# Optimization experiments

Hardware: AMD Instinct MI355X
Metric: run time of the kernel (lower is better)

The kernel has to match this reference:

```python
import jax, jax.numpy as jnp
import numpy as np

B, L, D_IN = 2048, 512, 32
PRED_LEN = 96
COND = 128      # cond_dim (z_dim)
XPROJ = 128     # x_proj_dim defaults to cond_dim
ODE_H = 128     # ode_hidden
TDIM = 128      # time_dim
HID = 256       # hidden of final MLP
N_STEPS = 32    # fixed-step RK4 steps over t in [0,1] (stands in for adaptive dopri5)
LN_EPS = 1e-5


def _linear(x, w, b):
    return x @ w.T + b


def _layernorm(x, g, b):
    mu = jnp.mean(x, axis=-1, keepdims=True)
    var = jnp.var(x, axis=-1, keepdims=True)
    return (x - mu) * jax.lax.rsqrt(var + LN_EPS) * g + b


def _interp(x_seq, t):
    # linear interp over sequence dim: x_seq (B,L,D), scalar t in [0,1] -> (B,D)
    Ls = x_seq.shape[1]
    pos = jnp.clip(t, 0.0, 1.0) * (Ls - 1)
    i0 = jnp.clip(jnp.floor(pos).astype(jnp.int32), 0, Ls - 1)
    i1 = jnp.clip(i0 + 1, 0, Ls - 1)
    w = (pos - i0.astype(pos.dtype))
    x0 = jax.lax.dynamic_index_in_dim(x_seq, i0, axis=1, keepdims=False)
    x1 = jax.lax.dynamic_index_in_dim(x_seq, i1, axis=1, keepdims=False)
    return (1.0 - w) * x0 + w * x1


def setup_inputs() -> dict:
    key = jax.random.key(0)
    ks = jax.random.split(key, 16)

    def kaiming(k, shape):
        return jax.random.normal(k, shape, jnp.float32) * np.float32(np.sqrt(2.0 / shape[-1]))

    IN_F = PRED_LEN * D_IN + COND + TDIM   # 3328
    OUT_F = PRED_LEN * D_IN                # 3072
    return {
        "x_t": jax.random.normal(ks[0], (B, PRED_LEN, D_IN), jnp.float32),
        "past": jax.random.normal(ks[1], (B, L, D_IN), jnp.float32),
        "t": jax.random.randint(ks[2], (B,), 0, 1000),
        "xproj_w": kaiming(ks[3], (XPROJ, D_IN)), "xproj_b": jnp.zeros((XPROJ,), jnp.float32),
        "z0_w": kaiming(ks[4], (COND, XPROJ)), "z0_b": jnp.zeros((COND,), jnp.float32),
        "ln_g": jnp.ones((COND,), jnp.float32), "ln_b": jnp.zeros((COND,), jnp.float32),
        "w1": kaiming(ks[5], (ODE_H, COND + XPROJ)), "b1": jnp.zeros((ODE_H,), jnp.float32),
        "w2": kaiming(ks[6], (ODE_H, ODE_H)), "b2": jnp.zeros((ODE_H,), jnp.float32),
        "w3": kaiming(ks[7], (COND, ODE_H)), "b3": jnp.zeros((COND,), jnp.float32),
        "fw1": kaiming(ks[8], (HID, IN_F)), "fb1": jnp.zeros((HID,), jnp.float32),
        "fw2": kaiming(ks[9], (HID, HID)), "fb2": jnp.zeros((HID,), jnp.float32),
        "fw3": kaiming(ks[10], (OUT_F, HID)), "fb3": jnp.zeros((OUT_F,), jnp.float32),
    }


def _time_emb(t):
    half = TDIM // 2
    freqs = jnp.exp(-np.float32(np.log(10000.0)) * jnp.arange(half, dtype=jnp.float32) / (half - 1))
    args = t.astype(jnp.float32)[:, None] * freqs[None, :]
    return jnp.concatenate([jnp.sin(args), jnp.cos(args)], axis=1)  # (B, TDIM)


def _forward(x_t, past, t, xproj_w, xproj_b, z0_w, z0_b, ln_g, ln_b,
             w1, b1, w2, b2, w3, b3, fw1, fb1, fw2, fb2, fw3, fb3):
    Bn = x_t.shape[0]
    x_seq = _linear(past, xproj_w, xproj_b)           # (B,L,XPROJ)
    z0 = _linear(x_seq[:, 0, :], z0_w, z0_b)          # (B,COND)

    def odef(tt, z):
        xt = _interp(x_seq, tt)                       # (B,XPROJ)
        zn = _layernorm(z, ln_g, ln_b)
        h = jnp.concatenate([zn, xt], axis=-1)
        h = jax.nn.silu(_linear(h, w1, b1))
        h = jax.nn.silu(_linear(h, w2, b2))
        return _linear(h, w3, b3)                     # (B,COND)

    dt = jnp.float32(1.0 / N_STEPS)

    def step(z, tt):
        k1 = odef(tt, z)
        k2 = odef(tt + dt * 0.5, z + dt * 0.5 * k1)
        k3 = odef(tt + dt * 0.5, z + dt * 0.5 * k2)
        k4 = odef(tt + dt, z + dt * k3)
        return z + (dt / 6.0) * (k1 + 2.0 * k2 + 2.0 * k3 + k4), None

    ts = jnp.arange(N_STEPS, dtype=jnp.float32) * dt
    cond, _ = jax.lax.scan(step, z0, ts)              # zT (B,COND)

    temb = _time_emb(t)                               # (B,TDIM)
    x_flat = x_t.reshape(Bn, -1)                      # (B,PRED_LEN*D_IN)
    h = jnp.concatenate([x_flat, cond, temb], axis=1)
    h = jax.nn.silu(_linear(h, fw1, fb1))
    h = jax.nn.silu(_linear(h, fw2, fb2))
    eps = _linear(h, fw3, fb3)
    return eps.reshape(Bn, PRED_LEN, D_IN)


def reference(x_t, past, t, xproj_w, xproj_b, z0_w, z0_b, ln_g, ln_b,
              w1, b1, w2, b2, w3, b3, fw1, fb1, fw2, fb2, fw3, fb3):
    return _forward(x_t, past, t, xproj_w, xproj_b, z0_w, z0_b, ln_g, ln_b,
                    w1, b1, w2, b2, w3, b3, fw1, fb1, fw2, fb2, fw3, fb3)
```

## Files before the change

kernel.cpp:

```cpp
#include <hip/hip_runtime.h>
#include <math.h>

typedef _Float16 h8f16 __attribute__((ext_vector_type(8)));
typedef _Float16 h4f16 __attribute__((ext_vector_type(4)));
typedef float f32x4 __attribute__((ext_vector_type(4)));

#define MFMA16(a, b, c) __builtin_amdgcn_mfma_f32_16x16x32_f16((a), (b), (c), 0, 0, 0)

__device__ __forceinline__ float silu_f(float v) {
    return v * __builtin_amdgcn_rcpf(1.0f + __expf(-v));
}

__global__ __launch_bounds__(128) void z0_kernel(
    const float* __restrict__ past,
    const float* __restrict__ xw, const float* __restrict__ xb,
    const float* __restrict__ zw, const float* __restrict__ zb,
    float* __restrict__ zbuf)
{
    __shared__ float p[32];
    __shared__ float x0[128];
    const int b = blockIdx.x;
    const int tid = threadIdx.x;
    if (tid < 32) p[tid] = past[(long)b * 512 * 32 + tid];
    __syncthreads();
    float s = xb[tid];
#pragma unroll
    for (int c = 0; c < 32; ++c) s += p[c] * xw[tid * 32 + c];
    x0[tid] = s;
    __syncthreads();
    float z = zb[tid];
    for (int k = 0; k < 128; ++k) z += x0[k] * zw[tid * 128 + k];
    zbuf[(long)b * 128 + tid] = z;
}

__global__ __launch_bounds__(256, 1) void ode_kernel(
    const float* __restrict__ past,
    const float* __restrict__ xproj_w, const float* __restrict__ xproj_b,
    const float* __restrict__ ln_g, const float* __restrict__ ln_b,
    const float* __restrict__ w1, const float* __restrict__ b1,
    const float* __restrict__ w2, const float* __restrict__ b2,
    const float* __restrict__ w3, const float* __restrict__ b3,
    float* __restrict__ zbuf)
{
    __shared__ _Float16 bxAll[65][16][40];
    __shared__ _Float16 hbuf[16][136];
    __shared__ _Float16 h1buf[16][136];
    __shared__ _Float16 h2buf[16][136];
    __shared__ float zS[16][132];
    __shared__ float kS[16][132];

    const int tid  = threadIdx.x;
    const int lane = tid & 63;
    const int wq   = tid >> 6;
    const int lrow = lane & 15;
    const int lhi  = lane >> 4;
    const int b0   = blockIdx.x * 16;

    h8f16 w1f[2][4], wcf[2], w2f[2][4], w3f[2][4];
    float b1t[2], b2r[2], b3r[2];
#pragma unroll
    for (int nt = 0; nt < 2; ++nt) {
        const int n = wq * 32 + nt * 16 + lrow;
#pragma unroll
        for (int ks = 0; ks < 4; ++ks) {
            const float* s = w1 + n * 256 + ks * 32 + lhi * 8;
            h8f16 v;
#pragma unroll
            for (int j = 0; j < 8; ++j) v[j] = (_Float16)s[j];
            w1f[nt][ks] = v;
        }
        {
            float wc[8] = {0, 0, 0, 0, 0, 0, 0, 0};
            float bc = 0.0f;
            const int c0 = lhi * 8;
            const float* w1b = w1 + n * 256 + 128;
#pragma unroll 4
            for (int k = 0; k < 128; ++k) {
                const float a = w1b[k];
                bc += a * xproj_b[k];
                const float* xr = xproj_w + k * 32 + c0;
#pragma unroll
                for (int j = 0; j < 8; ++j) wc[j] += a * xr[j];
            }
            h8f16 v;
#pragma unroll
            for (int j = 0; j < 8; ++j) v[j] = (_Float16)wc[j];
            wcf[nt] = v;
            b1t[nt] = b1[n] + bc;
        }
#pragma unroll
        for (int ks = 0; ks < 4; ++ks) {
            const float* s2 = w2 + n * 128 + ks * 32 + lhi * 8;
            const float* s3 = w3 + n * 128 + ks * 32 + lhi * 8;
            h8f16 v2, v3;
#pragma unroll
            for (int j = 0; j < 8; ++j) { v2[j] = (_Float16)s2[j]; v3[j] = (_Float16)s3[j]; }
            w2f[nt][ks] = v2; w3f[nt][ks] = v3;
        }
        b2r[nt] = b2[n]; b3r[nt] = b3[n];
    }

    const int r8 = tid >> 4;
    const int c8 = (tid & 15) * 8;
    float gR[8], bR[8];
#pragma unroll
    for (int j = 0; j < 8; ++j) { gR[j] = ln_g[c8 + j]; bR[j] = ln_b[c8 + j]; }

    for (int flat = tid; flat < 65 * 128; flat += 256) {
        const int e  = flat >> 7;
        const int u  = flat & 127;
        const int r  = u >> 3;
        const int c  = (u & 7) * 4;
        const float pos = (float)e * 7.984375f;
        const int i0 = (int)pos;
        const int i1 = (i0 < 511) ? i0 + 1 : 511;
        const float w = pos - (float)i0;
        const f32x4 a0 = *(const f32x4*)(past + ((long)(b0 + r) * 512 + i0) * 32 + c);
        const f32x4 a1 = *(const f32x4*)(past + ((long)(b0 + r) * 512 + i1) * 32 + c);
        h4f16 v;
#pragma unroll
        for (int j = 0; j < 4; ++j) v[j] = (_Float16)((1.0f - w) * a0[j] + w * a1[j]);
        *(h4f16*)&bxAll[e][r][c] = v;
    }

#pragma unroll
    for (int j = 0; j < 8; ++j) {
        zS[r8][c8 + j] = zbuf[(long)(b0 + r8) * 128 + c8 + j];
        kS[r8][c8 + j] = 0.0f;
    }

    f32x4 krk[2];
    krk[0] = (f32x4){0, 0, 0, 0}; krk[1] = (f32x4){0, 0, 0, 0};
    const float DT = 1.0f / 32.0f;

    __syncthreads();

#pragma unroll 1
    for (int step = 0; step < 32; ++step) {
#pragma unroll 1
        for (int sub = 0; sub < 4; ++sub) {
            const int e = 2 * step + ((sub + 1) >> 1);
            const float cin = (sub == 0) ? 0.0f : (sub == 3) ? DT : 0.5f * DT;

            {
                float x[8];
                float sum = 0.f, sq = 0.f;
#pragma unroll
                for (int j = 0; j < 8; ++j) {
                    float v = zS[r8][c8 + j] + cin * kS[r8][c8 + j];
                    x[j] = v; sum += v; sq += v * v;
                }
#pragma unroll
                for (int m = 1; m < 16; m <<= 1) {
                    sum += __shfl_xor(sum, m, 16);
                    sq  += __shfl_xor(sq,  m, 16);
                }
                const float mu  = sum * (1.0f / 128.0f);
                const float var = sq * (1.0f / 128.0f) - mu * mu;
                const float inv = 1.0f / sqrtf(var + 1e-5f);
                h8f16 o;
#pragma unroll
                for (int j = 0; j < 8; ++j)
                    o[j] = (_Float16)((x[j] - mu) * inv * gR[j] + bR[j]);
                *(h8f16*)&hbuf[r8][c8] = o;
            }
            __syncthreads();

            {
                h8f16 az[4];
#pragma unroll
                for (int ks = 0; ks < 4; ++ks)
                    az[ks] = *(const h8f16*)&hbuf[lrow][ks * 32 + lhi * 8];
                const h8f16 bx = *(const h8f16*)&bxAll[e][lrow][lhi * 8];
                f32x4 a0 = {0, 0, 0, 0}, a1 = {0, 0, 0, 0};
#pragma unroll
                for (int ks = 0; ks < 4; ++ks) {
                    a0 = MFMA16(az[ks], w1f[0][ks], a0);
                    a1 = MFMA16(az[ks], w1f[1][ks], a1);
                }
                a0 = MFMA16(bx, wcf[0], a0);
                a1 = MFMA16(bx, wcf[1], a1);
#pragma unroll
                for (int j = 0; j < 4; ++j) {
                    h1buf[lhi * 4 + j][wq * 32 + lrow]      = (_Float16)silu_f(a0[j] + b1t[0]);
                    h1buf[lhi * 4 + j][wq * 32 + 16 + lrow] = (_Float16)silu_f(a1[j] + b1t[1]);
                }
            }
            __syncthreads();

            {
                f32x4 a0 = {0, 0, 0, 0}, a1 = {0, 0, 0, 0};
#pragma unroll
                for (int ks = 0; ks < 4; ++ks) {
                    h8f16 a = *(const h8f16*)&h1buf[lrow][ks * 32 + lhi * 8];
                    a0 = MFMA16(a, w2f[0][ks], a0);
                    a1 = MFMA16(a, w2f[1][ks], a1);
                }
#pragma unroll
                for (int j = 0; j < 4; ++j) {
                    h2buf[lhi * 4 + j][wq * 32 + lrow]      = (_Float16)silu_f(a0[j] + b2r[0]);
                    h2buf[lhi * 4 + j][wq * 32 + 16 + lrow] = (_Float16)silu_f(a1[j] + b2r[1]);
                }
            }
            __syncthreads();

            {
                f32x4 a0 = {0, 0, 0, 0}, a1 = {0, 0, 0, 0};
#pragma unroll
                for (int ks = 0; ks < 4; ++ks) {
                    h8f16 a = *(const h8f16*)&h2buf[lrow][ks * 32 + lhi * 8];
                    a0 = MFMA16(a, w3f[0][ks], a0);
                    a1 = MFMA16(a, w3f[1][ks], a1);
                }
                if (sub < 3) {
                    const float wgt = (sub == 0) ? 1.0f : 2.0f;
#pragma unroll
                    for (int j = 0; j < 4; ++j) {
                        const float k0v = a0[j] + b3r[0];
                        const float k1v = a1[j] + b3r[1];
                        kS[lhi * 4 + j][wq * 32 + lrow]      = k0v;
                        kS[lhi * 4 + j][wq * 32 + 16 + lrow] = k1v;
                        if (sub == 0) { krk[0][j] = k0v;        krk[1][j] = k1v; }
                        else          { krk[0][j] += wgt * k0v; krk[1][j] += wgt * k1v; }
                    }
                } else {
#pragma unroll
                    for (int j = 0; j < 4; ++j) {
                        const float k0v = a0[j] + b3r[0];
                        const float k1v = a1[j] + b3r[1];
                        const int rr = lhi * 4 + j;
                        zS[rr][wq * 32 + lrow]      += (DT / 6.0f) * (krk[0][j] + k0v);
                        zS[rr][wq * 32 + 16 + lrow] += (DT / 6.0f) * (krk[1][j] + k1v);
                    }
                }
            }
            __syncthreads();
        }
    }

#pragma unroll
    for (int j = 0; j < 8; ++j)
        zbuf[(long)(b0 + r8) * 128 + c8 + j] = zS[r8][c8 + j];
}

__global__ __launch_bounds__(256) void hcat_kernel(
    const float* __restrict__ x_t, const float* __restrict__ cond,
    const int* __restrict__ tvals, _Float16* __restrict__ hcat)
{
    const int gid = blockIdx.x * 256 + threadIdx.x;
    const int b  = gid / 416;
    const int j0 = (gid % 416) * 8;
    h8f16 v;
    if (j0 < 3072) {
        const float* s = x_t + (long)b * 3072 + j0;
#pragma unroll
        for (int j = 0; j < 8; ++j) v[j] = (_Float16)s[j];
    } else if (j0 < 3200) {
        const float* s = cond + (long)b * 128 + (j0 - 3072);
#pragma unroll
        for (int j = 0; j < 8; ++j) v[j] = (_Float16)s[j];
    } else {
        const float tv = (float)tvals[b];
#pragma unroll
        for (int j = 0; j < 8; ++j) {
            const int jj  = j0 - 3200 + j;
            const int idx = (jj < 64) ? jj : jj - 64;
            const float fr = expf(-9.210340371976184f * (float)idx * (1.0f / 63.0f));
            const float a  = tv * fr;
            v[j] = (_Float16)((jj < 64) ? sinf(a) : cosf(a));
        }
    }
    *(h8f16*)&hcat[(long)b * 3328 + j0] = v;
}

template <bool SILU, bool OUT_F16>
__global__ __launch_bounds__(256) void gemm_f16(
    const _Float16* __restrict__ A, const float* __restrict__ W,
    const float* __restrict__ bias, void* __restrict__ out,
    int M, int N, int K)
{
    __shared__ _Float16 aS[64][40];
    __shared__ _Float16 wS[64][40];
    const int mb = blockIdx.x * 64, nb = blockIdx.y * 64;
    const int tid = threadIdx.x, lane = tid & 63, wq = tid >> 6;
    const int lrow = lane & 15, lhi = lane >> 4;
    f32x4 acc[4];
#pragma unroll
    for (int nt = 0; nt < 4; ++nt) acc[nt] = (f32x4){0, 0, 0, 0};

    const int sr = tid >> 2;
    const int sk = (tid & 3) * 8;

    for (int k0 = 0; k0 < K; k0 += 32) {
        {
            h8f16 v = *(const h8f16*)&A[(long)(mb + sr) * K + k0 + sk];
            *(h8f16*)&aS[sr][sk] = v;
        }
        {
            const float* s = &W[(long)(nb + sr) * K + k0 + sk];
            h8f16 v;
#pragma unroll
            for (int j = 0; j < 8; ++j) v[j] = (_Float16)s[j];
            *(h8f16*)&wS[sr][sk] = v;
        }
        __syncthreads();
        h8f16 a = *(const h8f16*)&aS[wq * 16 + lrow][lhi * 8];
#pragma unroll
        for (int nt = 0; nt < 4; ++nt) {
            h8f16 bfr = *(const h8f16*)&wS[nt * 16 + lrow][lhi * 8];
            acc[nt] = MFMA16(a, bfr, acc[nt]);
        }
        __syncthreads();
    }

#pragma unroll
    for (int nt = 0; nt < 4; ++nt) {
        const int cc = nb + nt * 16 + lrow;
        const float bv = bias[cc];
#pragma unroll
        for (int j = 0; j < 4; ++j) {
            const int rr = mb + wq * 16 + lhi * 4 + j;
            float v = acc[nt][j] + bv;
            if (SILU) v = silu_f(v);
            if (OUT_F16) ((_Float16*)out)[(long)rr * N + cc] = (_Float16)v;
            else         ((float*)out)[(long)rr * N + cc] = v;
        }
    }
}

extern "C" void kernel_launch(void* const* d_in, const int* in_sizes, int n_in,
                              void* d_out, int out_size, void* d_ws, size_t ws_size,
                              hipStream_t stream)
{
    const float* x_t     = (const float*)d_in[0];
    const float* past    = (const float*)d_in[1];
    const int*   tvals   = (const int*)d_in[2];
    const float* xproj_w = (const float*)d_in[3];
    const float* xproj_b = (const float*)d_in[4];
    const float* z0_w    = (const float*)d_in[5];
    const float* z0_b    = (const float*)d_in[6];
    const float* ln_g    = (const float*)d_in[7];
    const float* ln_b    = (const float*)d_in[8];
    const float* w1      = (const float*)d_in[9];
    const float* b1      = (const float*)d_in[10];
    const float* w2      = (const float*)d_in[11];
    const float* b2      = (const float*)d_in[12];
    const float* w3      = (const float*)d_in[13];
    const float* b3      = (const float*)d_in[14];
    const float* fw1     = (const float*)d_in[15];
    const float* fb1     = (const float*)d_in[16];
    const float* fw2     = (const float*)d_in[17];
    const float* fb2     = (const float*)d_in[18];
    const float* fw3     = (const float*)d_in[19];
    const float* fb3     = (const float*)d_in[20];

    char* ws = (char*)d_ws;
    float*     zbuf = (float*)ws;
    _Float16*  hcat = (_Float16*)(ws + (1 << 20));
    _Float16*  h1   = (_Float16*)(ws + 15 * (1 << 20));
    _Float16*  h2   = (_Float16*)(ws + 16 * (1 << 20));

    z0_kernel<<<2048, 128, 0, stream>>>(past, xproj_w, xproj_b, z0_w, z0_b, zbuf);

    ode_kernel<<<128, 256, 0, stream>>>(past, xproj_w, xproj_b, ln_g, ln_b,
                                        w1, b1, w2, b2, w3, b3, zbuf);

    hcat_kernel<<<(2048 * 416) / 256, 256, 0, stream>>>(x_t, zbuf, tvals, hcat);

    gemm_f16<true,  true ><<<dim3(32, 4),  256, 0, stream>>>(hcat, fw1, fb1, h1, 2048, 256, 3328);
    gemm_f16<true,  true ><<<dim3(32, 4),  256, 0, stream>>>(h1,   fw2, fb2, h2, 2048, 256, 256);
    gemm_f16<false, false><<<dim3(32, 48), 256, 0, stream>>>(h2,   fw3, fb3, d_out, 2048, 3072, 256);
}
```

Before: 335.7 us.

## Fuse LayerNorm into ODE MFMA stage and read x_t directly in first GEMM

In the ODE kernel, the RK4 state now lives in registers (zc) instead of shared memory. The next ODE input is written to a single XOR-swizzled shared buffer, and the LayerNorm is computed inside the first MFMA stage. That removes one barrier per sub-step, and the h1/h2 buffers are also swizzled to avoid bank conflicts. The hcat concatenation kernel is replaced by a small cond/time-embedding buffer, so the first GEMM converts x_t from fp32 on the fly and skips writing and re-reading a large fp16 activation. The trade-off is more register pressure and a duplicated LayerNorm reduction across waves.

New measurement: 434.7 us. +29.5%, slower.

```diff
diff --git a/kernel.cpp b/kernel.cpp
--- a/kernel.cpp
+++ b/kernel.cpp
@@ -43,11 +43,9 @@
     float* __restrict__ zbuf)
 {
     __shared__ _Float16 bxAll[65][16][40];
-    __shared__ _Float16 hbuf[16][136];
-    __shared__ _Float16 h1buf[16][136];
-    __shared__ _Float16 h2buf[16][136];
-    __shared__ float zS[16][132];
-    __shared__ float kS[16][132];
+    __shared__ float    vS[16 * 128];
+    __shared__ _Float16 h1S[16 * 128];
+    __shared__ _Float16 h2S[16 * 128];
 
     const int tid  = threadIdx.x;
     const int lane = tid & 63;
@@ -55,6 +53,7 @@
     const int lrow = lane & 15;
     const int lhi  = lane >> 4;
     const int b0   = blockIdx.x * 16;
+    const int rsw  = lrow & 7;
 
     h8f16 w1f[2][4], wcf[2], w2f[2][4], w3f[2][4];
     float b1t[2], b2r[2], b3r[2];
@@ -100,11 +99,14 @@
         b2r[nt] = b2[n]; b3r[nt] = b3[n];
     }
 
-    const int r8 = tid >> 4;
-    const int c8 = (tid & 15) * 8;
-    float gR[8], bR[8];
-#pragma unroll
-    for (int j = 0; j < 8; ++j) { gR[j] = ln_g[c8 + j]; bR[j] = ln_b[c8 + j]; }
+    float gln[4][8], bln[4][8];
+#pragma unroll
+    for (int ks = 0; ks < 4; ++ks)
+#pragma unroll
+        for (int j = 0; j < 8; ++j) {
+            gln[ks][j] = ln_g[ks * 32 + lhi * 8 + j];
+            bln[ks][j] = ln_b[ks * 32 + lhi * 8 + j];
+        }
 
     for (int flat = tid; flat < 65 * 128; flat += 256) {
         const int e  = flat >> 7;
@@ -123,10 +125,21 @@
         *(h4f16*)&bxAll[e][r][c] = v;
     }
 
-#pragma unroll
-    for (int j = 0; j < 8; ++j) {
-        zS[r8][c8 + j] = zbuf[(long)(b0 + r8) * 128 + c8 + j];
-        kS[r8][c8 + j] = 0.0f;
+    const int cA = wq * 32 + lrow, cB = cA + 16;
+    float zc[2][4];
+#pragma unroll
+    for (int j = 0; j < 4; ++j) {
+        const long rb = (long)(b0 + 4 * lhi + j) * 128;
+        zc[0][j] = zbuf[rb + cA];
+        zc[1][j] = zbuf[rb + cB];
+    }
+#pragma unroll
+    for (int j = 0; j < 4; ++j) {
+        const int row = 4 * lhi + j;
+        const int sA = row * 128 + (((cA >> 2) ^ (row & 7)) << 2) + (cA & 3);
+        const int sB = row * 128 + (((cB >> 2) ^ (row & 7)) << 2) + (cB & 3);
+        vS[sA] = zc[0][j];
+        vS[sB] = zc[1][j];
     }
 
     f32x4 krk[2];
@@ -140,37 +153,43 @@
 #pragma unroll 1
         for (int sub = 0; sub < 4; ++sub) {
             const int e = 2 * step + ((sub + 1) >> 1);
-            const float cin = (sub == 0) ? 0.0f : (sub == 3) ? DT : 0.5f * DT;
 
             {
-                float x[8];
-                float sum = 0.f, sq = 0.f;
-#pragma unroll
-                for (int j = 0; j < 8; ++j) {
-                    float v = zS[r8][c8 + j] + cin * kS[r8][c8 + j];
-                    x[j] = v; sum += v; sq += v * v;
-                }
-#pragma unroll
-                for (int m = 1; m < 16; m <<= 1) {
-                    sum += __shfl_xor(sum, m, 16);
-                    sq  += __shfl_xor(sq,  m, 16);
-                }
-                const float mu  = sum * (1.0f / 128.0f);
-                const float var = sq * (1.0f / 128.0f) - mu * mu;
+                f32x4 va[4][2];
+#pragma unroll
+                for (int ks = 0; ks < 4; ++ks) {
+                    const int bA = (8 * ks + 2 * lhi) ^ rsw;
+                    const int bB = (8 * ks + 2 * lhi + 1) ^ rsw;
+                    va[ks][0] = *(const f32x4*)&vS[lrow * 128 + (bA << 2)];
+                    va[ks][1] = *(const f32x4*)&vS[lrow * 128 + (bB << 2)];
+                }
+                float s = 0.f, q = 0.f;
+#pragma unroll
+                for (int ks = 0; ks < 4; ++ks)
+#pragma unroll
+                    for (int h = 0; h < 2; ++h)
+#pragma unroll
+                        for (int j = 0; j < 4; ++j) {
+                            const float v = va[ks][h][j];
+                            s += v; q += v * v;
+                        }
+                s += __shfl_xor(s, 16); q += __shfl_xor(q, 16);
+                s += __shfl_xor(s, 32); q += __shfl_xor(q, 32);
+                const float mu  = s * (1.0f / 128.0f);
+                const float var = q * (1.0f / 128.0f) - mu * mu;
                 const float inv = 1.0f / sqrtf(var + 1e-5f);
-                h8f16 o;
-#pragma unroll
-                for (int j = 0; j < 8; ++j)
-                    o[j] = (_Float16)((x[j] - mu) * inv * gR[j] + bR[j]);
-                *(h8f16*)&hbuf[r8][c8] = o;
-            }
-            __syncthreads();
-
-            {
+
                 h8f16 az[4];
 #pragma unroll
-                for (int ks = 0; ks < 4; ++ks)
-                    az[ks] = *(const h8f16*)&hbuf[lrow][ks * 32 + lhi * 8];
+                for (int ks = 0; ks < 4; ++ks) {
+                    h8f16 o;
+#pragma unroll
+                    for (int j = 0; j < 8; ++j) {
+                        const float v = va[ks][j >> 2][j & 3];
+                        o[j] = (_Float16)((v - mu) * inv * gln[ks][j] + bln[ks][j]);
+                    }
+                    az[ks] = o;
+                }
                 const h8f16 bx = *(const h8f16*)&bxAll[e][lrow][lhi * 8];
                 f32x4 a0 = {0, 0, 0, 0}, a1 = {0, 0, 0, 0};
 #pragma unroll
@@ -182,8 +201,11 @@
                 a1 = MFMA16(bx, wcf[1], a1);
 #pragma unroll
                 for (int j = 0; j < 4; ++j) {
-                    h1buf[lhi * 4 + j][wq * 32 + lrow]      = (_Float16)silu_f(a0[j] + b1t[0]);
-                    h1buf[lhi * 4 + j][wq * 32 + 16 + lrow] = (_Float16)silu_f(a1[j] + b1t[1]);
+                    const int row = 4 * lhi + j;
+                    const int pA = row * 128 + ((((cA >> 3) ^ (row & 7)) << 3)) + (cA & 7);
+                    const int pB = row * 128 + ((((cB >> 3) ^ (row & 7)) << 3)) + (cB & 7);
+                    h1S[pA] = (_Float16)silu_f(a0[j] + b1t[0]);
+                    h1S[pB] = (_Float16)silu_f(a1[j] + b1t[1]);
                 }
             }
             __syncthreads();
@@ -192,14 +214,18 @@
                 f32x4 a0 = {0, 0, 0, 0}, a1 = {0, 0, 0, 0};
 #pragma unroll
                 for (int ks = 0; ks < 4; ++ks) {
-                    h8f16 a = *(const h8f16*)&h1buf[lrow][ks * 32 + lhi * 8];
+                    const int blk = (4 * ks + lhi) ^ rsw;
+                    h8f16 a = *(const h8f16*)&h1S[lrow * 128 + (blk << 3)];
                     a0 = MFMA16(a, w2f[0][ks], a0);
                     a1 = MFMA16(a, w2f[1][ks], a1);
                 }
 #pragma unroll
                 for (int j = 0; j < 4; ++j) {
-                    h2buf[lhi * 4 + j][wq * 32 + lrow]      = (_Float16)silu_f(a0[j] + b2r[0]);
-                    h2buf[lhi * 4 + j][wq * 32 + 16 + lrow] = (_Float16)silu_f(a1[j] + b2r[1]);
+                    const int row = 4 * lhi + j;
+                    const int pA = row * 128 + ((((cA >> 3) ^ (row & 7)) << 3)) + (cA & 7);
+                    const int pB = row * 128 + ((((cB >> 3) ^ (row & 7)) << 3)) + (cB & 7);
+                    h2S[pA] = (_Float16)silu_f(a0[j] + b2r[0]);
+                    h2S[pB] = (_Float16)silu_f(a1[j] + b2r[1]);
                 }
             }
             __syncthreads();
@@ -208,30 +234,39 @@
                 f32x4 a0 = {0, 0, 0, 0}, a1 = {0, 0, 0, 0};
 #pragma unroll
                 for (int ks = 0; ks < 4; ++ks) {
-                    h8f16 a = *(const h8f16*)&h2buf[lrow][ks * 32 + lhi * 8];
+                    const int blk = (4 * ks + lhi) ^ rsw;
+                    h8f16 a = *(const h8f16*)&h2S[lrow * 128 + (blk << 3)];
                     a0 = MFMA16(a, w3f[0][ks], a0);
                     a1 = MFMA16(a, w3f[1][ks], a1);
                 }
-                if (sub < 3) {
-                    const float wgt = (sub == 0) ? 1.0f : 2.0f;
-#pragma unroll
-                    for (int j = 0; j < 4; ++j) {
-                        const float k0v = a0[j] + b3r[0];
-                        const float k1v = a1[j] + b3r[1];
-                        kS[lhi * 4 + j][wq * 32 + lrow]      = k0v;
-                        kS[lhi * 4 + j][wq * 32 + 16 + lrow] = k1v;
-                        if (sub == 0) { krk[0][j] = k0v;        krk[1][j] = k1v; }
-                        else          { krk[0][j] += wgt * k0v; krk[1][j] += wgt * k1v; }
+#pragma unroll
+                for (int j = 0; j < 4; ++j) {
+                    const float k0v = a0[j] + b3r[0];
+                    const float k1v = a1[j] + b3r[1];
+                    float v0, v1;
+                    if (sub == 0) {
+                        krk[0][j] = k0v; krk[1][j] = k1v;
+                        v0 = zc[0][j] + 0.5f * DT * k0v;
+                        v1 = zc[1][j] + 0.5f * DT * k1v;
+                    } else if (sub == 1) {
+                        krk[0][j] += 2.0f * k0v; krk[1][j] += 2.0f * k1v;
+                        v0 = zc[0][j] + 0.5f * DT * k0v;
+                        v1 = zc[1][j] + 0.5f * DT * k1v;
+                    } else if (sub == 2) {
+                        krk[0][j] += 2.0f * k0v; krk[1][j] += 2.0f * k1v;
+                        v0 = zc[0][j] + DT * k0v;
+                        v1 = zc[1][j] + DT * k1v;
+                    } else {
+                        zc[0][j] += (DT / 6.0f) * (krk[0][j] + k0v);
+                        zc[1][j] += (DT / 6.0f) * (krk[1][j] + k1v);
+                        v0 = zc[0][j];
+                        v1 = zc[1][j];
                     }
-                } else {
-#pragma unroll
-                    for (int j = 0; j < 4; ++j) {
-                        const float k0v = a0[j] + b3r[0];
-                        const float k1v = a1[j] + b3r[1];
-                        const int rr = lhi * 4 + j;
-                        zS[rr][wq * 32 + lrow]      += (DT / 6.0f) * (krk[0][j] + k0v);
-                        zS[rr][wq * 32 + 16 + lrow] += (DT / 6.0f) * (krk[1][j] + k1v);
-                    }
+                    const int row = 4 * lhi + j;
+                    const int sA = row * 128 + (((cA >> 2) ^ (row & 7)) << 2) + (cA & 3);
+                    const int sB = row * 128 + (((cB >> 2) ^ (row & 7)) << 2) + (cB & 3);
+                    vS[sA] = v0;
+                    vS[sB] = v1;
                 }
             }
             __syncthreads();
@@ -239,38 +274,95 @@
     }
 
 #pragma unroll
-    for (int j = 0; j < 8; ++j)
-        zbuf[(long)(b0 + r8) * 128 + c8 + j] = zS[r8][c8 + j];
-}
-
-__global__ __launch_bounds__(256) void hcat_kernel(
-    const float* __restrict__ x_t, const float* __restrict__ cond,
-    const int* __restrict__ tvals, _Float16* __restrict__ hcat)
+    for (int j = 0; j < 4; ++j) {
+        const long rb = (long)(b0 + 4 * lhi + j) * 128;
+        zbuf[rb + cA] = zc[0][j];
+        zbuf[rb + cB] = zc[1][j];
+    }
+}
+
+__global__ __launch_bounds__(256) void cbuf_kernel(
+    const float* __restrict__ cond, const int* __restrict__ tvals,
+    _Float16* __restrict__ cbuf)
 {
     const int gid = blockIdx.x * 256 + threadIdx.x;
-    const int b  = gid / 416;
-    const int j0 = (gid % 416) * 8;
+    const int b  = gid >> 5;
+    const int j0 = (gid & 31) * 8;
     h8f16 v;
-    if (j0 < 3072) {
-        const float* s = x_t + (long)b * 3072 + j0;
-#pragma unroll
-        for (int j = 0; j < 8; ++j) v[j] = (_Float16)s[j];
-    } else if (j0 < 3200) {
-        const float* s = cond + (long)b * 128 + (j0 - 3072);
+    if (j0 < 128) {
+        const float* s = cond + (long)b * 128 + j0;
 #pragma unroll
         for (int j = 0; j < 8; ++j) v[j] = (_Float16)s[j];
     } else {
         const float tv = (float)tvals[b];
 #pragma unroll
         for (int j = 0; j < 8; ++j) {
-            const int jj  = j0 - 3200 + j;
+            const int jj  = j0 - 128 + j;
             const int idx = (jj < 64) ? jj : jj - 64;
             const float fr = expf(-9.210340371976184f * (float)idx * (1.0f / 63.0f));
             const float a  = tv * fr;
             v[j] = (_Float16)((jj < 64) ? sinf(a) : cosf(a));
         }
     }
-    *(h8f16*)&hcat[(long)b * 3328 + j0] = v;
+    *(h8f16*)&cbuf[(long)b * 256 + j0] = v;
+}
+
+__global__ __launch_bounds__(256) void gemm1_kernel(
+    const float* __restrict__ x_t, const _Float16* __restrict__ cbuf,
+    const float* __restrict__ W, const float* __restrict__ bias,
+    _Float16* __restrict__ out)
+{
+    const int M = 2048, N = 256, K = 3328;
+    __shared__ _Float16 aS[64][40];
+    __shared__ _Float16 wS[64][40];
+    const int mb = blockIdx.x * 64, nb = blockIdx.y * 64;
+    const int tid = threadIdx.x, lane = tid & 63, wq = tid >> 6;
+    const int lrow = lane & 15, lhi = lane >> 4;
+    f32x4 acc[4];
+#pragma unroll
+    for (int nt = 0; nt < 4; ++nt) acc[nt] = (f32x4){0, 0, 0, 0};
+
+    const int sr = tid >> 2;
+    const int sk = (tid & 3) * 8;
+
+    for (int k0 = 0; k0 < K; k0 += 32) {
+        if (k0 < 3072) {
+            const float* s = x_t + (long)(mb + sr) * 3072 + k0 + sk;
+            h8f16 v;
+#pragma unroll
+            for (int j = 0; j < 8; ++j) v[j] = (_Float16)s[j];
+            *(h8f16*)&aS[sr][sk] = v;
+        } else {
+            *(h8f16*)&aS[sr][sk] =
+                *(const h8f16*)&cbuf[(long)(mb + sr) * 256 + (k0 - 3072) + sk];
+        }
+        {
+            const float* s = &W[(long)(nb + sr) * K + k0 + sk];
+            h8f16 v;
+#pragma unroll
+            for (int j = 0; j < 8; ++j) v[j] = (_Float16)s[j];
+            *(h8f16*)&wS[sr][sk] = v;
+        }
+        __syncthreads();
+        h8f16 a = *(const h8f16*)&aS[wq * 16 + lrow][lhi * 8];
+#pragma unroll
+        for (int nt = 0; nt < 4; ++nt) {
+            h8f16 bfr = *(const h8f16*)&wS[nt * 16 + lrow][lhi * 8];
+            acc[nt] = MFMA16(a, bfr, acc[nt]);
+        }
+        __syncthreads();
+    }
+
+#pragma unroll
+    for (int nt = 0; nt < 4; ++nt) {
+        const int cc = nb + nt * 16 + lrow;
+        const float bv = bias[cc];
+#pragma unroll
+        for (int j = 0; j < 4; ++j) {
+            const int rr = mb + wq * 16 + lhi * 4 + j;
+            out[(long)rr * N + cc] = (_Float16)silu_f(acc[nt][j] + bv);
+        }
+    }
 }
 
 template <bool SILU, bool OUT_F16>
@@ -356,18 +448,18 @@
 
     char* ws = (char*)d_ws;
     float*     zbuf = (float*)ws;
-    _Float16*  hcat = (_Float16*)(ws + (1 << 20));
-    _Float16*  h1   = (_Float16*)(ws + 15 * (1 << 20));
-    _Float16*  h2   = (_Float16*)(ws + 16 * (1 << 20));
+    _Float16*  cbuf = (_Float16*)(ws + (1 << 20));
+    _Float16*  h1   = (_Float16*)(ws + 2 * (1 << 20));
+    _Float16*  h2   = (_Float16*)(ws + 3 * (1 << 20));
 
     z0_kernel<<<2048, 128, 0, stream>>>(past, xproj_w, xproj_b, z0_w, z0_b, zbuf);
 
     ode_kernel<<<128, 256, 0, stream>>>(past, xproj_w, xproj_b, ln_g, ln_b,
                                         w1, b1, w2, b2, w3, b3, zbuf);
 
-    hcat_kernel<<<(2048 * 416) / 256, 256, 0, stream>>>(x_t, zbuf, tvals, hcat);
-
-    gemm_f16<true,  true ><<<dim3(32, 4),  256, 0, stream>>>(hcat, fw1, fb1, h1, 2048, 256, 3328);
-    gemm_f16<true,  true ><<<dim3(32, 4),  256, 0, stream>>>(h1,   fw2, fb2, h2, 2048, 256, 256);
-    gemm_f16<false, false><<<dim3(32, 48), 256, 0, stream>>>(h2,   fw3, fb3, d_out, 2048, 3072, 256);
-}
+    cbuf_kernel<<<256, 256, 0, stream>>>(zbuf, tvals, cbuf);
+
+    gemm1_kernel<<<dim3(32, 4), 256, 0, stream>>>(x_t, cbuf, fw1, fb1, h1);
+    gemm_f16<true,  true ><<<dim3(32, 4),  256, 0, stream>>>(h1, fw2, fb2, h2, 2048, 256, 256);
+    gemm_f16<false, false><<<dim3(32, 48), 256, 0, stream>>>(h2, fw3, fb3, d_out, 2048, 3072, 256);
+}
```

## Fuse z0 into ODE kernel, widen to 8 waves, fold LN affine into W1

Applied to the files above, without the earlier changes.

The z0 projection kernel is merged into the ODE kernel, so one launch disappears. The block grows to 512 threads so each wave owns 16 output columns instead of 32, which halves the MFMA chain per wave. LayerNorm gamma/beta are folded into W1 and its bias, and normalisation is applied in fp16 on MFMA operands read straight from hbuf, which removes the separate LN phase and one barrier per substep. The state z and the RK accumulators now live in registers. The interpolated past rows are prefetched from global one substep ahead instead of being staged all at once into shared memory. The trade-offs are more fp16 rounding in the normalisation and the z0 work running on only 128 blocks.

After: 372.3 us. +10.9%, slower.

```diff
diff --git a/kernel.cpp b/kernel.cpp
--- a/kernel.cpp
+++ b/kernel.cpp
@@ -2,7 +2,6 @@
 #include <math.h>
 
 typedef _Float16 h8f16 __attribute__((ext_vector_type(8)));
-typedef _Float16 h4f16 __attribute__((ext_vector_type(4)));
 typedef float f32x4 __attribute__((ext_vector_type(4)));
 
 #define MFMA16(a, b, c) __builtin_amdgcn_mfma_f32_16x16x32_f16((a), (b), (c), 0, 0, 0)
@@ -11,236 +10,248 @@
     return v * __builtin_amdgcn_rcpf(1.0f + __expf(-v));
 }
 
-__global__ __launch_bounds__(128) void z0_kernel(
-    const float* __restrict__ past,
-    const float* __restrict__ xw, const float* __restrict__ xb,
-    const float* __restrict__ zw, const float* __restrict__ zb,
-    float* __restrict__ zbuf)
-{
-    __shared__ float p[32];
-    __shared__ float x0[128];
-    const int b = blockIdx.x;
-    const int tid = threadIdx.x;
-    if (tid < 32) p[tid] = past[(long)b * 512 * 32 + tid];
-    __syncthreads();
-    float s = xb[tid];
-#pragma unroll
-    for (int c = 0; c < 32; ++c) s += p[c] * xw[tid * 32 + c];
-    x0[tid] = s;
-    __syncthreads();
-    float z = zb[tid];
-    for (int k = 0; k < 128; ++k) z += x0[k] * zw[tid * 128 + k];
-    zbuf[(long)b * 128 + tid] = z;
-}
-
-__global__ __launch_bounds__(256, 1) void ode_kernel(
+__global__ __launch_bounds__(512, 1) void ode_kernel(
     const float* __restrict__ past,
     const float* __restrict__ xproj_w, const float* __restrict__ xproj_b,
+    const float* __restrict__ z0_w, const float* __restrict__ z0_b,
     const float* __restrict__ ln_g, const float* __restrict__ ln_b,
     const float* __restrict__ w1, const float* __restrict__ b1,
     const float* __restrict__ w2, const float* __restrict__ b2,
     const float* __restrict__ w3, const float* __restrict__ b3,
     float* __restrict__ zbuf)
 {
-    __shared__ _Float16 bxAll[65][16][40];
     __shared__ _Float16 hbuf[16][136];
-    __shared__ _Float16 h1buf[16][136];
-    __shared__ _Float16 h2buf[16][136];
-    __shared__ float zS[16][132];
-    __shared__ float kS[16][132];
+    __shared__ _Float16 h1S[16][136];
+    __shared__ _Float16 h2S[16][136];
+    __shared__ float    pS[16][33];
+    __shared__ float    x0S[16][128];
+    __shared__ float    zS0[16][129];
 
     const int tid  = threadIdx.x;
+    const int wid  = tid >> 6;
     const int lane = tid & 63;
-    const int wq   = tid >> 6;
     const int lrow = lane & 15;
     const int lhi  = lane >> 4;
     const int b0   = blockIdx.x * 16;
-
-    h8f16 w1f[2][4], wcf[2], w2f[2][4], w3f[2][4];
-    float b1t[2], b2r[2], b3r[2];
-#pragma unroll
-    for (int nt = 0; nt < 2; ++nt) {
-        const int n = wq * 32 + nt * 16 + lrow;
+    const int nc   = wid * 16 + lrow;
+    const int koff = lhi * 8;
+
+    h8f16 w1f[4], wcf, w2f[4], w3f[4];
+    float b1t, b2r, b3r;
+    {
 #pragma unroll
         for (int ks = 0; ks < 4; ++ks) {
-            const float* s = w1 + n * 256 + ks * 32 + lhi * 8;
-            h8f16 v;
-#pragma unroll
-            for (int j = 0; j < 8; ++j) v[j] = (_Float16)s[j];
-            w1f[nt][ks] = v;
-        }
-        {
-            float wc[8] = {0, 0, 0, 0, 0, 0, 0, 0};
-            float bc = 0.0f;
-            const int c0 = lhi * 8;
-            const float* w1b = w1 + n * 256 + 128;
+            h8f16 v1, v2, v3;
+#pragma unroll
+            for (int j = 0; j < 8; ++j) {
+                const int k = ks * 32 + koff + j;
+                v1[j] = (_Float16)(w1[nc * 256 + k] * ln_g[k]);
+                v2[j] = (_Float16)w2[nc * 128 + k];
+                v3[j] = (_Float16)w3[nc * 128 + k];
+            }
+            w1f[ks] = v1; w2f[ks] = v2; w3f[ks] = v3;
+        }
+        float wc[8] = {0, 0, 0, 0, 0, 0, 0, 0};
+        float bc = 0.0f, bb = 0.0f;
+        const float* w1a = w1 + nc * 256;
+        const float* w1b = w1a + 128;
 #pragma unroll 4
-            for (int k = 0; k < 128; ++k) {
-                const float a = w1b[k];
-                bc += a * xproj_b[k];
-                const float* xr = xproj_w + k * 32 + c0;
-#pragma unroll
-                for (int j = 0; j < 8; ++j) wc[j] += a * xr[j];
-            }
-            h8f16 v;
-#pragma unroll
-            for (int j = 0; j < 8; ++j) v[j] = (_Float16)wc[j];
-            wcf[nt] = v;
-            b1t[nt] = b1[n] + bc;
-        }
-#pragma unroll
-        for (int ks = 0; ks < 4; ++ks) {
-            const float* s2 = w2 + n * 128 + ks * 32 + lhi * 8;
-            const float* s3 = w3 + n * 128 + ks * 32 + lhi * 8;
-            h8f16 v2, v3;
-#pragma unroll
-            for (int j = 0; j < 8; ++j) { v2[j] = (_Float16)s2[j]; v3[j] = (_Float16)s3[j]; }
-            w2f[nt][ks] = v2; w3f[nt][ks] = v3;
-        }
-        b2r[nt] = b2[n]; b3r[nt] = b3[n];
-    }
-
-    const int r8 = tid >> 4;
-    const int c8 = (tid & 15) * 8;
-    float gR[8], bR[8];
-#pragma unroll
-    for (int j = 0; j < 8; ++j) { gR[j] = ln_g[c8 + j]; bR[j] = ln_b[c8 + j]; }
-
-    for (int flat = tid; flat < 65 * 128; flat += 256) {
-        const int e  = flat >> 7;
-        const int u  = flat & 127;
-        const int r  = u >> 3;
-        const int c  = (u & 7) * 4;
+        for (int k = 0; k < 128; ++k) {
+            const float a = w1b[k];
+            bc += a * xproj_b[k];
+            bb += w1a[k] * ln_b[k];
+            const float* xr = xproj_w + k * 32 + koff;
+#pragma unroll
+            for (int j = 0; j < 8; ++j) wc[j] += a * xr[j];
+        }
+        h8f16 v;
+#pragma unroll
+        for (int j = 0; j < 8; ++j) v[j] = (_Float16)wc[j];
+        wcf = v;
+        b1t = b1[nc] + bc + bb;
+        b2r = b2[nc]; b3r = b3[nc];
+    }
+
+    pS[tid >> 5][tid & 31] = past[(long)(b0 + (tid >> 5)) * 16384 + (tid & 31)];
+    __syncthreads();
+    {
+        const int r  = tid >> 5;
+        const int c0 = (tid & 31) * 4;
+#pragma unroll
+        for (int cc = 0; cc < 4; ++cc) {
+            const int kc = c0 + cc;
+            float s = xproj_b[kc];
+            const float* xr = xproj_w + kc * 32;
+#pragma unroll
+            for (int c = 0; c < 32; ++c) s += pS[r][c] * xr[c];
+            x0S[r][kc] = s;
+        }
+    }
+    __syncthreads();
+    {
+        const int nn = tid & 127;
+        const int r0 = (tid >> 7) * 4;
+        for (int p = 0; p < 4; ++p) {
+            const int r = r0 + p;
+            float s = z0_b[nn];
+            const float* zr = z0_w + nn * 128;
+            for (int k = 0; k < 128; ++k) s += x0S[r][k] * zr[k];
+            zS0[r][nn] = s;
+        }
+    }
+    __syncthreads();
+
+    float zc[4], krk[4];
+#pragma unroll
+    for (int j = 0; j < 4; ++j) {
+        zc[j] = zS0[4 * lhi + j][nc];
+        hbuf[4 * lhi + j][nc] = (_Float16)zc[j];
+    }
+
+    const float DT = 1.0f / 32.0f;
+
+    f32x4 s0a, s0b, s1a, s1b;
+    auto stage = [&](int e) {
         const float pos = (float)e * 7.984375f;
         const int i0 = (int)pos;
         const int i1 = (i0 < 511) ? i0 + 1 : 511;
-        const float w = pos - (float)i0;
-        const f32x4 a0 = *(const f32x4*)(past + ((long)(b0 + r) * 512 + i0) * 32 + c);
-        const f32x4 a1 = *(const f32x4*)(past + ((long)(b0 + r) * 512 + i1) * 32 + c);
-        h4f16 v;
-#pragma unroll
-        for (int j = 0; j < 4; ++j) v[j] = (_Float16)((1.0f - w) * a0[j] + w * a1[j]);
-        *(h4f16*)&bxAll[e][r][c] = v;
-    }
-
-#pragma unroll
-    for (int j = 0; j < 8; ++j) {
-        zS[r8][c8 + j] = zbuf[(long)(b0 + r8) * 128 + c8 + j];
-        kS[r8][c8 + j] = 0.0f;
-    }
-
-    f32x4 krk[2];
-    krk[0] = (f32x4){0, 0, 0, 0}; krk[1] = (f32x4){0, 0, 0, 0};
-    const float DT = 1.0f / 32.0f;
-
+        const float* base = past + (long)(b0 + lrow) * 16384;
+        const float* p0 = base + i0 * 32 + koff;
+        const float* p1 = base + i1 * 32 + koff;
+        s0a = *(const f32x4*)p0; s0b = *(const f32x4*)(p0 + 4);
+        s1a = *(const f32x4*)p1; s1b = *(const f32x4*)(p1 + 4);
+    };
+    auto blend = [&](int e) -> h8f16 {
+        const float pos = (float)e * 7.984375f;
+        const float w = pos - floorf(pos);
+        h8f16 r;
+#pragma unroll
+        for (int j = 0; j < 4; ++j) {
+            r[j]     = (_Float16)(s0a[j] + w * (s1a[j] - s0a[j]));
+            r[4 + j] = (_Float16)(s0b[j] + w * (s1b[j] - s0b[j]));
+        }
+        return r;
+    };
+
+    auto phaseA = [&](h8f16 bxc) {
+        h8f16 xf[4];
+#pragma unroll
+        for (int ks = 0; ks < 4; ++ks)
+            xf[ks] = *(const h8f16*)&hbuf[lrow][ks * 32 + koff];
+        float s = 0.f, q = 0.f;
+#pragma unroll
+        for (int ks = 0; ks < 4; ++ks)
+#pragma unroll
+            for (int j = 0; j < 8; ++j) {
+                const float v = (float)xf[ks][j];
+                s += v; q = fmaf(v, v, q);
+            }
+        s += __shfl_xor(s, 16); q += __shfl_xor(q, 16);
+        s += __shfl_xor(s, 32); q += __shfl_xor(q, 32);
+        const float mu  = s * (1.0f / 128.0f);
+        const float var = q * (1.0f / 128.0f) - mu * mu;
+        const float inv = 1.0f / sqrtf(var + 1e-5f);
+        const _Float16 ih = (_Float16)inv;
+        const _Float16 mh = (_Float16)(-mu * inv);
+        h8f16 ip, mp;
+#pragma unroll
+        for (int j = 0; j < 8; ++j) { ip[j] = ih; mp[j] = mh; }
+        f32x4 acc = {0, 0, 0, 0};
+#pragma unroll
+        for (int ks = 0; ks < 4; ++ks) {
+            const h8f16 az = xf[ks] * ip + mp;
+            acc = MFMA16(az, w1f[ks], acc);
+        }
+        acc = MFMA16(bxc, wcf, acc);
+#pragma unroll
+        for (int j = 0; j < 4; ++j)
+            h1S[4 * lhi + j][nc] = (_Float16)silu_f(acc[j] + b1t);
+    };
+    auto phaseB = [&]() {
+        f32x4 acc = {0, 0, 0, 0};
+#pragma unroll
+        for (int ks = 0; ks < 4; ++ks) {
+            const h8f16 a = *(const h8f16*)&h1S[lrow][ks * 32 + koff];
+            acc = MFMA16(a, w2f[ks], acc);
+        }
+#pragma unroll
+        for (int j = 0; j < 4; ++j)
+            h2S[4 * lhi + j][nc] = (_Float16)silu_f(acc[j] + b2r);
+    };
+    auto phaseC = [&]() -> f32x4 {
+        f32x4 acc = {0, 0, 0, 0};
+#pragma unroll
+        for (int ks = 0; ks < 4; ++ks) {
+            const h8f16 a = *(const h8f16*)&h2S[lrow][ks * 32 + koff];
+            acc = MFMA16(a, w3f[ks], acc);
+        }
+#pragma unroll
+        for (int j = 0; j < 4; ++j) acc[j] += b3r;
+        return acc;
+    };
+
+    stage(0);
+    h8f16 bxc = blend(0);
     __syncthreads();
 
 #pragma unroll 1
-    for (int step = 0; step < 32; ++step) {
-#pragma unroll 1
-        for (int sub = 0; sub < 4; ++sub) {
-            const int e = 2 * step + ((sub + 1) >> 1);
-            const float cin = (sub == 0) ? 0.0f : (sub == 3) ? DT : 0.5f * DT;
-
-            {
-                float x[8];
-                float sum = 0.f, sq = 0.f;
-#pragma unroll
-                for (int j = 0; j < 8; ++j) {
-                    float v = zS[r8][c8 + j] + cin * kS[r8][c8 + j];
-                    x[j] = v; sum += v; sq += v * v;
-                }
-#pragma unroll
-                for (int m = 1; m < 16; m <<= 1) {
-                    sum += __shfl_xor(sum, m, 16);
-                    sq  += __shfl_xor(sq,  m, 16);
-                }
-                const float mu  = sum * (1.0f / 128.0f);
-                const float var = sq * (1.0f / 128.0f) - mu * mu;
-                const float inv = 1.0f / sqrtf(var + 1e-5f);
-                h8f16 o;
-#pragma unroll
-                for (int j = 0; j < 8; ++j)
-                    o[j] = (_Float16)((x[j] - mu) * inv * gR[j] + bR[j]);
-                *(h8f16*)&hbuf[r8][c8] = o;
-            }
-            __syncthreads();
-
-            {
-                h8f16 az[4];
-#pragma unroll
-                for (int ks = 0; ks < 4; ++ks)
-                    az[ks] = *(const h8f16*)&hbuf[lrow][ks * 32 + lhi * 8];
-                const h8f16 bx = *(const h8f16*)&bxAll[e][lrow][lhi * 8];
-                f32x4 a0 = {0, 0, 0, 0}, a1 = {0, 0, 0, 0};
-#pragma unroll
-                for (int ks = 0; ks < 4; ++ks) {
-                    a0 = MFMA16(az[ks], w1f[0][ks], a0);
-                    a1 = MFMA16(az[ks], w1f[1][ks], a1);
-                }
-                a0 = MFMA16(bx, wcf[0], a0);
-                a1 = MFMA16(bx, wcf[1], a1);
-#pragma unroll
-                for (int j = 0; j < 4; ++j) {
-                    h1buf[lhi * 4 + j][wq * 32 + lrow]      = (_Float16)silu_f(a0[j] + b1t[0]);
-                    h1buf[lhi * 4 + j][wq * 32 + 16 + lrow] = (_Float16)silu_f(a1[j] + b1t[1]);
-                }
-            }
-            __syncthreads();
-
-            {
-                f32x4 a0 = {0, 0, 0, 0}, a1 = {0, 0, 0, 0};
-#pragma unroll
-                for (int ks = 0; ks < 4; ++ks) {
-                    h8f16 a = *(const h8f16*)&h1buf[lrow][ks * 32 + lhi * 8];
-                    a0 = MFMA16(a, w2f[0][ks], a0);
-                    a1 = MFMA16(a, w2f[1][ks], a1);
-                }
-#pragma unroll
-                for (int j = 0; j < 4; ++j) {
-                    h2buf[lhi * 4 + j][wq * 32 + lrow]      = (_Float16)silu_f(a0[j] + b2r[0]);
-                    h2buf[lhi * 4 + j][wq * 32 + 16 + lrow] = (_Float16)silu_f(a1[j] + b2r[1]);
-                }
-            }
-            __syncthreads();
-
-            {
-                f32x4 a0 = {0, 0, 0, 0}, a1 = {0, 0, 0, 0};
-#pragma unroll
-                for (int ks = 0; ks < 4; ++ks) {
-                    h8f16 a = *(const h8f16*)&h2buf[lrow][ks * 32 + lhi * 8];
-                    a0 = MFMA16(a, w3f[0][ks], a0);
-                    a1 = MFMA16(a, w3f[1][ks], a1);
-                }
-                if (sub < 3) {
-                    const float wgt = (sub == 0) ? 1.0f : 2.0f;
-#pragma unroll
-                    for (int j = 0; j < 4; ++j) {
-                        const float k0v = a0[j] + b3r[0];
-                        const float k1v = a1[j] + b3r[1];
-                        kS[lhi * 4 + j][wq * 32 + lrow]      = k0v;
-                        kS[lhi * 4 + j][wq * 32 + 16 + lrow] = k1v;
-                        if (sub == 0) { krk[0][j] = k0v;        krk[1][j] = k1v; }
-                        else          { krk[0][j] += wgt * k0v; krk[1][j] += wgt * k1v; }
-                    }
-                } else {
-#pragma unroll
-                    for (int j = 0; j < 4; ++j) {
-                        const float k0v = a0[j] + b3r[0];
-                        const float k1v = a1[j] + b3r[1];
-                        const int rr = lhi * 4 + j;
-                        zS[rr][wq * 32 + lrow]      += (DT / 6.0f) * (krk[0][j] + k0v);
-                        zS[rr][wq * 32 + 16 + lrow] += (DT / 6.0f) * (krk[1][j] + k1v);
-                    }
-                }
-            }
-            __syncthreads();
-        }
-    }
-
-#pragma unroll
-    for (int j = 0; j < 8; ++j)
-        zbuf[(long)(b0 + r8) * 128 + c8 + j] = zS[r8][c8 + j];
+    for (int st = 0; st < 32; ++st) {
+        const int e1 = 2 * st + 1, e2 = 2 * st + 2;
+        phaseA(bxc);
+        stage(e1);
+        __syncthreads();
+        phaseB(); __syncthreads();
+        {
+            const f32x4 k = phaseC();
+#pragma unroll
+            for (int j = 0; j < 4; ++j) {
+                krk[j] = k[j];
+                hbuf[4 * lhi + j][nc] = (_Float16)(zc[j] + 0.5f * DT * k[j]);
+            }
+        }
+        __syncthreads();
+        bxc = blend(e1);
+        phaseA(bxc); __syncthreads();
+        phaseB(); __syncthreads();
+        {
+            const f32x4 k = phaseC();
+#pragma unroll
+            for (int j = 0; j < 4; ++j) {
+                krk[j] += 2.0f * k[j];
+                hbuf[4 * lhi + j][nc] = (_Float16)(zc[j] + 0.5f * DT * k[j]);
+            }
+        }
+        __syncthreads();
+        phaseA(bxc);
+        stage(e2);
+        __syncthreads();
+        phaseB(); __syncthreads();
+        {
+            const f32x4 k = phaseC();
+#pragma unroll
+            for (int j = 0; j < 4; ++j) {
+                krk[j] += 2.0f * k[j];
+                hbuf[4 * lhi + j][nc] = (_Float16)(zc[j] + DT * k[j]);
+            }
+        }
+        __syncthreads();
+        bxc = blend(e2);
+        phaseA(bxc); __syncthreads();
+        phaseB(); __syncthreads();
+        {
+            const f32x4 k = phaseC();
+#pragma unroll
+            for (int j = 0; j < 4; ++j) {
+                zc[j] += (DT / 6.0f) * (krk[j] + k[j]);
+                hbuf[4 * lhi + j][nc] = (_Float16)zc[j];
+            }
+        }
+        __syncthreads();
+    }
+
+#pragma unroll
+    for (int j = 0; j < 4; ++j)
+        zbuf[(long)(b0 + 4 * lhi + j) * 128 + nc] = zc[j];
 }
 
 __global__ __launch_bounds__(256) void hcat_kernel(
@@ -360,10 +371,8 @@
     _Float16*  h1   = (_Float16*)(ws + 15 * (1 << 20));
     _Float16*  h2   = (_Float16*)(ws + 16 * (1 << 20));
 
-    z0_kernel<<<2048, 128, 0, stream>>>(past, xproj_w, xproj_b, z0_w, z0_b, zbuf);
-
-    ode_kernel<<<128, 256, 0, stream>>>(past, xproj_w, xproj_b, ln_g, ln_b,
-                                        w1, b1, w2, b2, w3, b3, zbuf);
+    ode_kernel<<<128, 512, 0, stream>>>(past, xproj_w, xproj_b, z0_w, z0_b,
+                                        ln_g, ln_b, w1, b1, w2, b2, w3, b3, zbuf);
 
     hcat_kernel<<<(2048 * 416) / 256, 256, 0, stream>>>(x_t, zbuf, tvals, hcat);
 
```
